# Kernel tuning notes

Hardware: AMD Instinct MI355X
Metric: run time of the kernel (lower is better)

## Reference

```python
import jax, jax.numpy as jnp
import numpy as np

DIM = 768
D_STATE = 16
D_INNER = 2 * DIM  # expand=2


def setup_inputs() -> dict:
    key = jax.random.key(0)
    k_x, k_in, k_conv, k_out = jax.random.split(key, 4)
    B, L = 1, 4096
    x = jax.random.normal(k_x, (B, L, DIM), dtype=jnp.float32)
    # torch Linear weight layout: [out_features, in_features]
    W_in = jax.random.normal(k_in, (3 * D_INNER + 2 * D_STATE, DIM), dtype=jnp.float32) * 0.02
    # depthwise conv1d kernel: [out_ch=d_inner, in_ch/groups=1, k=3]
    W_conv = jax.random.normal(k_conv, (D_INNER, 1, 3), dtype=jnp.float32) * 0.1
    W_out = jax.random.normal(k_out, (DIM, D_INNER), dtype=jnp.float32) * 0.02
    A_log = jnp.log(jnp.tile(jnp.arange(1, D_STATE + 1, dtype=jnp.float32), (D_INNER, 1)))
    D = jnp.ones((D_INNER,), dtype=jnp.float32)
    return {"x": x, "W_in": W_in, "W_conv": W_conv, "W_out": W_out, "A_log": A_log, "D": D}


def reference(x, W_in, W_conv, W_out, A_log, D):
    d_inner = W_conv.shape[0]
    d_state = A_log.shape[1]
    Bsz = x.shape[0]

    xz = x @ W_in.T  # [B, L, 3*d_inner + 2*d_state]
    x_inner, z, B_ssm, C_ssm, delta = jnp.split(
        xz, [d_inner, 2 * d_inner, 2 * d_inner + d_state, 2 * d_inner + 2 * d_state], axis=-1
    )

    # depthwise conv over sequence: [B, d_inner, L]
    xc = jax.lax.conv_general_dilated(
        x_inner.transpose(0, 2, 1), W_conv,
        window_strides=(1,), padding=[(1, 1)], feature_group_count=d_inner,
    ).transpose(0, 2, 1)  # back to [B, L, d_inner]
    xc = jax.nn.silu(xc)

    A = -jnp.exp(A_log)  # [d_inner, d_state]
    delta = jax.nn.softplus(delta)  # [B, L, d_inner]
    dA = jnp.exp(jnp.einsum('bld,dn->bldn', delta, A))           # [B, L, d_inner, d_state]
    dBx = jnp.einsum('bld,bln,bld->bldn', delta, B_ssm, xc)      # delta_B * x fused

    def step(h, inp):
        da_t, dbx_t, c_t = inp  # [B,d,n], [B,d,n], [B,n]
        h = da_t * h + dbx_t
        y_t = jnp.einsum('bdn,bn->bd', h, c_t)
        return h, y_t

    h0 = jnp.zeros((Bsz, d_inner, d_state), dtype=x.dtype)
    _, ys = jax.lax.scan(
        step, h0,
        (dA.transpose(1, 0, 2, 3), dBx.transpose(1, 0, 2, 3), C_ssm.transpose(1, 0, 2)),
    )  # ys: [L, B, d_inner]

    y = ys.transpose(1, 0, 2) + xc * D  # skip connection
    y = y * jax.nn.silu(z)
    return y @ W_out.T  # [B, L, dim]
```

## Files before the change

kernel.cpp:

```cpp
#include <hip/hip_runtime.h>
#include <hip/hip_bf16.h>
#include <math.h>

#define LSEQ   4096
#define DIM    768
#define DINNER 1536
#define DSTATE 16
#define NCOLS  4640
#define NCH    128
#define CLEN   32
#define NPAD   4736
#define DXW    1568

typedef _Float16 f16;
typedef __attribute__((ext_vector_type(8))) _Float16 f16x8;
typedef __attribute__((ext_vector_type(4))) float f32x4;

__device__ __forceinline__ void gld_lds16(void* lds_dst, const void* gsrc) {
    __builtin_amdgcn_global_load_lds(
        (__attribute__((address_space(1))) void*)(gsrc),
        (__attribute__((address_space(3))) void*)(lds_dst), 16, 0, 0);
}

template<int BM, int BN, int WM, int WN, int NTB, bool COLM, bool ZMODE>
__global__ __launch_bounds__(256) void gemm_f16(const f16* __restrict__ A,
                                                const f16* __restrict__ B,
                                                float* __restrict__ C,
                                                f16* __restrict__ Xb,
                                                f16* __restrict__ Zb,
                                                int M, int N, int K, int ldc) {
    constexpr int MI  = WM / 16;
    constexpr int NI  = WN / 16;
    constexpr int NWN = BN / WN;
    constexpr int RT  = BM + BN;
    constexpr int NS  = RT / 8;

    __shared__ __align__(16) f16 S[RT * 64];
    f16* As = S;
    f16* Bs = S + BM * 64;

    const int P   = gridDim.x >> 3;
    const int idx = (blockIdx.x & 7) * P + (blockIdx.x >> 3);
    const int m0  = (COLM ? (idx % NTB) : (idx / NTB)) * BM;
    const int n0  = (COLM ? (idx / NTB) : (idx % NTB)) * BN;

    const int tid  = threadIdx.x;
    const int w    = tid >> 6;
    const int lane = tid & 63;
    const int wr   = w / NWN;
    const int wc   = w % NWN;
    const int m    = lane & 15;
    const int q    = lane >> 4;
    const int rl8  = lane >> 3;
    const int bsel = lane & 7;

    f32x4 acc[MI][NI];
#pragma unroll
    for (int i = 0; i < MI; i++)
#pragma unroll
        for (int j = 0; j < NI; j++) acc[i][j] = (f32x4){0.f, 0.f, 0.f, 0.f};

    for (int k0 = 0; k0 < K; k0 += 64) {
#pragma unroll
        for (int t = w; t < NS; t += 4) {
            const int rl  = t * 8 + rl8;
            const int blk = bsel ^ (rl & 7);
            const f16* g = (rl < BM)
                ? A + (size_t)(m0 + rl) * K + k0 + blk * 8
                : B + (size_t)(n0 + rl - BM) * K + k0 + blk * 8;
            gld_lds16(S + t * 8 * 64, g);
        }
        __syncthreads();

#pragma unroll
        for (int kk = 0; kk < 2; kk++) {
            const int fo = (((q + 4 * kk) ^ (m & 7)) << 3);
            f16x8 af[MI], bh[NI];
#pragma unroll
            for (int i = 0; i < MI; i++)
                af[i] = *(const f16x8*)&As[(wr * WM + i * 16 + m) * 64 + fo];
#pragma unroll
            for (int j = 0; j < NI; j++)
                bh[j] = *(const f16x8*)&Bs[(wc * WN + j * 16 + m) * 64 + fo];
#pragma unroll
            for (int i = 0; i < MI; i++)
#pragma unroll
                for (int j = 0; j < NI; j++)
                    acc[i][j] = __builtin_amdgcn_mfma_f32_16x16x32_f16(
                        af[i], bh[j], acc[i][j], 0, 0, 0);
        }
        __syncthreads();
    }

    if (ZMODE && n0 < DINNER) {
#pragma unroll
        for (int i = 0; i < MI; i++)
#pragma unroll
            for (int j = 0; j < NI; j++) {
                const int col  = n0 + wc * WN + j * 16 + m;
                const int rowb = m0 + wr * WM + i * 16 + q * 4;
#pragma unroll
                for (int r = 0; r < 4; r++)
                    Xb[(size_t)(rowb + r) * DINNER + col] = (f16)acc[i][j][r];
            }
        return;
    }
    if (ZMODE && n0 < 2 * DINNER) {
#pragma unroll
        for (int i = 0; i < MI; i++)
#pragma unroll
            for (int j = 0; j < NI; j++) {
                const int col  = n0 - DINNER + wc * WN + j * 16 + m;
                const int rowb = m0 + wr * WM + i * 16 + q * 4;
#pragma unroll
                for (int r = 0; r < 4; r++)
                    Zb[(size_t)(rowb + r) * DINNER + col] = (f16)acc[i][j][r];
            }
        return;
    }
#pragma unroll
    for (int i = 0; i < MI; i++)
#pragma unroll
        for (int j = 0; j < NI; j++) {
            const int col  = (ZMODE ? n0 - 2 * DINNER : n0) + wc * WN + j * 16 + m;
            const int lim  = ZMODE ? DXW : N;
            if (col >= lim) continue;
            const int rowb = m0 + wr * WM + i * 16 + q * 4;
#pragma unroll
            for (int r = 0; r < 4; r++)
                C[(size_t)(rowb + r) * ldc + col] = acc[i][j][r];
        }
}

#define E0 (LSEQ * DIM)
#define E1 (E0 + NPAD * DIM)
#define E2 (E1 + DIM * DINNER)

__global__ __launch_bounds__(256) void cvt_all(const float* __restrict__ x,
                                               const float* __restrict__ Wi,
                                               const float* __restrict__ Wo,
                                               f16* __restrict__ Ax,
                                               f16* __restrict__ Bw,
                                               f16* __restrict__ Bo) {
    int i = (blockIdx.x * 256 + threadIdx.x) * 4;
    if (i < E0) {
        float4 v = *(const float4*)(x + i);
        Ax[i] = (f16)v.x; Ax[i+1] = (f16)v.y; Ax[i+2] = (f16)v.z; Ax[i+3] = (f16)v.w;
    } else if (i < E1) {
        int e = i - E0;
        int n = e / DIM;
        if (n < NCOLS) {
            float4 v = *(const float4*)(Wi + e);
            Bw[e] = (f16)v.x; Bw[e+1] = (f16)v.y; Bw[e+2] = (f16)v.z; Bw[e+3] = (f16)v.w;
        } else {
            Bw[e] = (f16)0.f; Bw[e+1] = (f16)0.f; Bw[e+2] = (f16)0.f; Bw[e+3] = (f16)0.f;
        }
    } else if (i < E2) {
        int e = i - E1;
        float4 v = *(const float4*)(Wo + e);
        Bo[e] = (f16)v.x; Bo[e+1] = (f16)v.y; Bo[e+2] = (f16)v.z; Bo[e+3] = (f16)v.w;
    }
}

__global__ __launch_bounds__(256) void scan1_kernel(const float* __restrict__ Dxz,
                                                    const f16* __restrict__ Xb,
                                                    const float* __restrict__ Wc,
                                                    const float* __restrict__ A_log,
                                                    float* __restrict__ aprod,
                                                    float* __restrict__ hend) {
    __shared__ float Bs[CLEN * DSTATE];
    const int d  = blockIdx.x * 256 + threadIdx.x;
    const int c  = blockIdx.y;
    const int l0 = c * CLEN;
    for (int i = threadIdx.x; i < CLEN * DSTATE; i += 256)
        Bs[i] = Dxz[(size_t)(l0 + (i >> 4)) * DXW + (i & 15)];
    float Areg[DSTATE];
#pragma unroll
    for (int n = 0; n < DSTATE; n++) Areg[n] = -__expf(A_log[d * DSTATE + n]);
    const float w0 = Wc[d * 3 + 0], w1 = Wc[d * 3 + 1], w2 = Wc[d * 3 + 2];
    float xm = (l0 > 0) ? (float)Xb[(size_t)(l0 - 1) * DINNER + d] : 0.f;
    float x0 = (float)Xb[(size_t)l0 * DINNER + d];
    float ld_xp   = (float)Xb[(size_t)(l0 + 1) * DINNER + d];
    float ld_draw = Dxz[(size_t)l0 * DXW + 32 + d];
    __syncthreads();

    float h[DSTATE];
#pragma unroll
    for (int n = 0; n < DSTATE; n++) h[n] = 0.f;
    float S = 0.f;

    for (int t = 0; t < CLEN; t++) {
        const int l = l0 + t;
        float xp = ld_xp, draw = ld_draw;
        if (t + 1 < CLEN) {
            ld_xp   = (l + 2 < LSEQ) ? (float)Xb[(size_t)(l + 2) * DINNER + d] : 0.f;
            ld_draw = Dxz[(size_t)(l + 1) * DXW + 32 + d];
        }
        float v  = xm * w0 + x0 * w1 + xp * w2;
        float xcv = __fdividef(v, 1.f + __expf(-v));
        float dtv = (draw > 20.f) ? draw : __logf(1.f + __expf(draw));
        float u = dtv * xcv;
        S += dtv;
#pragma unroll
        for (int n = 0; n < DSTATE; n++) {
            float e = __expf(dtv * Areg[n]);
            h[n] = e * h[n] + u * Bs[t * DSTATE + n];
        }
        xm = x0; x0 = xp;
    }
#pragma unroll
    for (int n = 0; n < DSTATE; n++) {
        size_t idx = ((size_t)c * DSTATE + n) * DINNER + d;
        aprod[idx] = __expf(S * Areg[n]);
        hend[idx]  = h[n];
    }
}

__global__ __launch_bounds__(256) void scan2_kernel(const float* __restrict__ aprod,
                                                    const float* __restrict__ hend,
                                                    float* __restrict__ hinit) {
    const int g = blockIdx.x * 256 + threadIdx.x;
    const size_t S = (size_t)DSTATE * DINNER;
    size_t idx = g;
    float a = aprod[idx], e = hend[idx];
    float h = 0.f;
#pragma unroll 4
    for (int c = 0; c < NCH; c++) {
        float ac = a, ec = e;
        if (c + 1 < NCH) { a = aprod[idx + S]; e = hend[idx + S]; }
        hinit[idx] = h;
        h = ac * h + ec;
        idx += S;
    }
}

__global__ __launch_bounds__(256) void scan3_kernel(const float* __restrict__ Dxz,
                                                    const f16* __restrict__ Xb,
                                                    const f16* __restrict__ Zb,
                                                    const float* __restrict__ Wc,
                                                    const float* __restrict__ A_log,
                                                    const float* __restrict__ hinit,
                                                    const float* __restrict__ Dp,
                                                    f16* __restrict__ Ay) {
    __shared__ float Bs[CLEN * DSTATE];
    __shared__ float Cs[CLEN * DSTATE];
    const int d  = blockIdx.x * 256 + threadIdx.x;
    const int c  = blockIdx.y;
    const int l0 = c * CLEN;
    for (int i = threadIdx.x; i < CLEN * DSTATE; i += 256) {
        size_t roff = (size_t)(l0 + (i >> 4)) * DXW;
        Bs[i] = Dxz[roff + (i & 15)];
        Cs[i] = Dxz[roff + 16 + (i & 15)];
    }
    float Areg[DSTATE];
#pragma unroll
    for (int n = 0; n < DSTATE; n++) Areg[n] = -__expf(A_log[d * DSTATE + n]);
    float h[DSTATE];
#pragma unroll
    for (int n = 0; n < DSTATE; n++)
        h[n] = hinit[((size_t)c * DSTATE + n) * DINNER + d];
    const float Dv = Dp[d];
    const float w0 = Wc[d * 3 + 0], w1 = Wc[d * 3 + 1], w2 = Wc[d * 3 + 2];
    float xm = (l0 > 0) ? (float)Xb[(size_t)(l0 - 1) * DINNER + d] : 0.f;
    float x0 = (float)Xb[(size_t)l0 * DINNER + d];
    float ld_xp   = (float)Xb[(size_t)(l0 + 1) * DINNER + d];
    float ld_draw = Dxz[(size_t)l0 * DXW + 32 + d];
    float ld_z    = (float)Zb[(size_t)l0 * DINNER + d];
    __syncthreads();

    for (int t = 0; t < CLEN; t++) {
        const int l = l0 + t;
        float xp = ld_xp, draw = ld_draw, zv = ld_z;
        if (t + 1 < CLEN) {
            ld_xp   = (l + 2 < LSEQ) ? (float)Xb[(size_t)(l + 2) * DINNER + d] : 0.f;
            ld_draw = Dxz[(size_t)(l + 1) * DXW + 32 + d];
            ld_z    = (float)Zb[(size_t)(l + 1) * DINNER + d];
        }
        float v  = xm * w0 + x0 * w1 + xp * w2;
        float xcv = __fdividef(v, 1.f + __expf(-v));
        float dtv = (draw > 20.f) ? draw : __logf(1.f + __expf(draw));
        float u = dtv * xcv;
        float y = 0.f;
#pragma unroll
        for (int n = 0; n < DSTATE; n++) {
            float e = __expf(dtv * Areg[n]);
            h[n] = e * h[n] + u * Bs[t * DSTATE + n];
            y += h[n] * Cs[t * DSTATE + n];
        }
        float sz = __fdividef(zv, 1.f + __expf(-zv));
        Ay[(size_t)l * DINNER + d] = (f16)((y + xcv * Dv) * sz);
        xm = x0; x0 = xp;
    }
}

extern "C" void kernel_launch(void* const* d_in, const int* in_sizes, int n_in,
                              void* d_out, int out_size, void* d_ws, size_t ws_size,
                              hipStream_t stream) {
    const float* x     = (const float*)d_in[0];
    const float* W_in  = (const float*)d_in[1];
    const float* W_conv= (const float*)d_in[2];
    const float* W_out = (const float*)d_in[3];
    const float* A_log = (const float*)d_in[4];
    const float* Dp    = (const float*)d_in[5];
    float* out = (float*)d_out;

    float* ws  = (float*)d_ws;
    float* Dxz = ws;
    float* ap  = Dxz + (size_t)LSEQ * DXW;
    float* he  = ap + (size_t)NCH * DSTATE * DINNER;
    float* hi  = he + (size_t)NCH * DSTATE * DINNER;
    f16* Ax = (f16*)(hi + (size_t)NCH * DSTATE * DINNER);
    f16* Ay = Ax + (size_t)LSEQ * DIM;
    f16* Bw = Ay + (size_t)LSEQ * DINNER;
    f16* Bo = Bw + (size_t)NPAD * DIM;
    f16* Zb = Bo + (size_t)DIM * DINNER;
    f16* Xb = Zb + (size_t)LSEQ * DINNER;

    cvt_all<<<E2 / 1024, 256, 0, stream>>>(x, W_in, W_out, Ax, Bw, Bo);

    gemm_f16<128, 128, 64, 64, 32, true, true><<<1184, 256, 0, stream>>>(
        Ax, Bw, Dxz, Xb, Zb, LSEQ, NCOLS, DIM, DXW);

    scan1_kernel<<<dim3(DINNER / 256, NCH), 256, 0, stream>>>(
        Dxz, Xb, W_conv, A_log, ap, he);
    scan2_kernel<<<(DINNER * DSTATE) / 256, 256, 0, stream>>>(ap, he, hi);
    scan3_kernel<<<dim3(DINNER / 256, NCH), 256, 0, stream>>>(
        Dxz, Xb, Zb, W_conv, A_log, hi, Dp, Ay);

    gemm_f16<64, 64, 32, 32, 12, false, false><<<768, 256, 0, stream>>>(
        Ay, Bo, out, nullptr, nullptr, LSEQ, DIM, DINNER, DIM);
}
```

Baseline: 242.8 us.

## Replace input-projection GEMM with triple-buffered 256x128 tile, 512-thread pipelined kernel

Adds a dedicated kernel for the input projection GEMM. It uses 256x128 tiles, 8 waves, and a three-stage LDS ring fed by direct global-to-LDS loads, with vmcnt-based waits so the next tiles load while MFMAs run. It also remaps blocks with an XCD-aware swizzle and raises wave priority around the MFMA section. The goal is to hide memory latency and improve reuse over the older generic 128x128 kernel. In exchange it uses much more LDS per block (about 144KB), which limits occupancy, and it drops bounds checks, relying on the fixed problem sizes.

```diff
diff --git a/kernel.cpp b/kernel.cpp
--- a/kernel.cpp
+++ b/kernel.cpp
@@ -20,6 +20,129 @@
     __builtin_amdgcn_global_load_lds(
         (__attribute__((address_space(1))) void*)(gsrc),
         (__attribute__((address_space(3))) void*)(lds_dst), 16, 0, 0);
+}
+
+#define G1K    768
+#define G1_NT  12
+#define G1_BM  256
+#define G1_BN  128
+#define G1_RT  384
+#define G1_LDSE (G1_RT * 64)
+
+__global__ __launch_bounds__(512) void gemm1_pipe(const f16* __restrict__ A,
+                                                  const f16* __restrict__ B,
+                                                  float* __restrict__ C,
+                                                  f16* __restrict__ Xb,
+                                                  f16* __restrict__ Zb) {
+    __shared__ __align__(16) f16 S[3 * G1_LDSE];
+
+    const int P   = gridDim.x >> 3;
+    const int idx = (blockIdx.x & 7) * P + (blockIdx.x >> 3);
+    const int m0  = (idx & 15) * G1_BM;
+    const int n0  = (idx >> 4) * G1_BN;
+
+    const int tid  = threadIdx.x;
+    const int w    = tid >> 6;
+    const int lane = tid & 63;
+    const int wr   = w >> 1;
+    const int wc   = w & 1;
+    const int m    = lane & 15;
+    const int q    = lane >> 4;
+    const int rl8  = lane >> 3;
+    const int bsel = lane & 7;
+
+    const f16* gb[6];
+#pragma unroll
+    for (int s = 0; s < 6; ++s) {
+        const int rl  = (w + 8 * s) * 8 + rl8;
+        const int blk = bsel ^ (rl & 7);
+        gb[s] = (rl < G1_BM) ? A + (size_t)(m0 + rl) * G1K + blk * 8
+                             : B + (size_t)(n0 + rl - G1_BM) * G1K + blk * 8;
+    }
+
+    f32x4 acc[4][4];
+#pragma unroll
+    for (int i = 0; i < 4; i++)
+#pragma unroll
+        for (int j = 0; j < 4; j++) acc[i][j] = (f32x4){0.f, 0.f, 0.f, 0.f};
+
+    auto stg = [&](int kt) {
+        f16* dst = S + (kt % 3) * G1_LDSE;
+#pragma unroll
+        for (int s = 0; s < 6; ++s)
+            gld_lds16(dst + (w + 8 * s) * 512, gb[s] + kt * 64);
+    };
+
+    stg(0);
+    stg(1);
+
+#pragma unroll
+    for (int kt = 0; kt < G1_NT; ++kt) {
+        if (kt < G1_NT - 1) asm volatile("s_waitcnt vmcnt(6)" ::: "memory");
+        else                asm volatile("s_waitcnt vmcnt(0)" ::: "memory");
+        __builtin_amdgcn_s_barrier();
+        if (kt + 2 < G1_NT) stg(kt + 2);
+
+        const f16* As = S + (kt % 3) * G1_LDSE;
+        const f16* Bs = As + G1_BM * 64;
+        __builtin_amdgcn_s_setprio(1);
+#pragma unroll
+        for (int kk = 0; kk < 2; kk++) {
+            const int fo = (((q + 4 * kk) ^ (m & 7)) << 3);
+            f16x8 af[4], bh[4];
+#pragma unroll
+            for (int i = 0; i < 4; i++)
+                af[i] = *(const f16x8*)&As[(wr * 64 + i * 16 + m) * 64 + fo];
+#pragma unroll
+            for (int j = 0; j < 4; j++)
+                bh[j] = *(const f16x8*)&Bs[(wc * 64 + j * 16 + m) * 64 + fo];
+#pragma unroll
+            for (int i = 0; i < 4; i++)
+#pragma unroll
+                for (int j = 0; j < 4; j++)
+                    acc[i][j] = __builtin_amdgcn_mfma_f32_16x16x32_f16(
+                        af[i], bh[j], acc[i][j], 0, 0, 0);
+        }
+        __builtin_amdgcn_s_setprio(0);
+    }
+
+    if (n0 < DINNER) {
+#pragma unroll
+        for (int i = 0; i < 4; i++)
+#pragma unroll
+            for (int j = 0; j < 4; j++) {
+                const int col  = n0 + wc * 64 + j * 16 + m;
+                const int rowb = m0 + wr * 64 + i * 16 + q * 4;
+#pragma unroll
+                for (int r = 0; r < 4; r++)
+                    Xb[(size_t)(rowb + r) * DINNER + col] = (f16)acc[i][j][r];
+            }
+        return;
+    }
+    if (n0 < 2 * DINNER) {
+#pragma unroll
+        for (int i = 0; i < 4; i++)
+#pragma unroll
+            for (int j = 0; j < 4; j++) {
+                const int col  = n0 - DINNER + wc * 64 + j * 16 + m;
+                const int rowb = m0 + wr * 64 + i * 16 + q * 4;
+#pragma unroll
+                for (int r = 0; r < 4; r++)
+                    Zb[(size_t)(rowb + r) * DINNER + col] = (f16)acc[i][j][r];
+            }
+        return;
+    }
+#pragma unroll
+    for (int i = 0; i < 4; i++)
+#pragma unroll
+        for (int j = 0; j < 4; j++) {
+            const int col = n0 - 2 * DINNER + wc * 64 + j * 16 + m;
+            if (col >= DXW) continue;
+            const int rowb = m0 + wr * 64 + i * 16 + q * 4;
+#pragma unroll
+            for (int r = 0; r < 4; r++)
+                C[(size_t)(rowb + r) * DXW + col] = acc[i][j][r];
+        }
 }
 
 template<int BM, int BN, int WM, int WN, int NTB, bool COLM, bool ZMODE>
@@ -318,8 +441,7 @@
 
     cvt_all<<<E2 / 1024, 256, 0, stream>>>(x, W_in, W_out, Ax, Bw, Bo);
 
-    gemm_f16<128, 128, 64, 64, 32, true, true><<<1184, 256, 0, stream>>>(
-        Ax, Bw, Dxz, Xb, Zb, LSEQ, NCOLS, DIM, DXW);
+    gemm1_pipe<<<592, 512, 0, stream>>>(Ax, Bw, Dxz, Xb, Zb);
 
     scan1_kernel<<<dim3(DINNER / 256, NCH), 256, 0, stream>>>(
         Dxz, Xb, W_conv, A_log, ap, he);
```

After: 245.1 us. Within noise of the previous version (+0.9%).
